# Kernel optimization log

Hardware: AMD Instinct MI355X
Metric: run time of the kernel (lower is better)

## Reference

```python
import jax, jax.numpy as jnp
import numpy as np

N = 50000      # nodes
E = 800000     # edges
F = 128        # num_features
H = 128        # hidden_channels
L = 3          # num_layers
P = 32         # num_partitions
EPS = 1e-5     # BatchNorm1d eps


def _batchnorm(h):
    # BatchNorm1d(affine=False, track_running_stats=False): batch stats, biased var
    m = jnp.mean(h, axis=0)
    v = jnp.var(h, axis=0)
    return (h - m) * jax.lax.rsqrt(v + EPS)


def setup_inputs() -> dict:
    key = jax.random.key(0)
    ks = jax.random.split(key, 12)
    x = jax.random.normal(ks[0], (N, F), dtype=jnp.float32)
    edge_index = jax.random.randint(ks[1], (2, E), 0, N)
    edge_weights = jax.random.uniform(ks[2], (E,), dtype=jnp.float32)
    partitions = (jax.random.uniform(ks[3], (N, P)) < (1.0 / P)).astype(jnp.float32)
    node_weights = jax.random.uniform(ks[4], (N,), dtype=jnp.float32)
    edge_curr_node = jax.random.uniform(ks[5], (N,), dtype=jnp.float32)
    conv_w = 0.05 * jax.random.normal(ks[6], (L, F, H), dtype=jnp.float32)
    conv_b = jnp.zeros((L, H), dtype=jnp.float32)
    lin1_w = 0.05 * jax.random.normal(ks[7], (4 * H, H), dtype=jnp.float32)
    lin1_b = jnp.zeros((H,), dtype=jnp.float32)
    lin2_w = 0.05 * jax.random.normal(ks[8], (H, 1), dtype=jnp.float32)
    lin2_b = jnp.zeros((1,), dtype=jnp.float32)
    return {"x": x, "edge_index": edge_index, "edge_weights": edge_weights,
            "partitions": partitions, "node_weights": node_weights,
            "edge_curr_node": edge_curr_node, "conv_w": conv_w, "conv_b": conv_b,
            "lin1_w": lin1_w, "lin1_b": lin1_b, "lin2_w": lin2_w,
            "lin2_b": lin2_b, "curr_node_id": 123}


def reference(x, edge_index, edge_weights, partitions, node_weights,
              edge_curr_node, conv_w, conv_b, lin1_w, lin1_b, lin2_w, lin2_b,
              curr_node_id):
    src, dst = edge_index[0], edge_index[1]
    # GCN normalization with added self-loops (weight 1)
    deg = jax.ops.segment_sum(edge_weights, dst, num_segments=N) + 1.0
    dinv = jax.lax.rsqrt(deg)
    norm = dinv[src] * edge_weights * dinv[dst]          # [E]
    self_norm = (dinv * dinv)[:, None]                   # [N,1]

    h = x
    for l in range(L):
        hw = h @ conv_w[l] + conv_b[l]                   # [N,H]
        agg = jax.ops.segment_sum(hw[src] * norm[:, None], dst, num_segments=N)
        agg = agg + hw * self_norm                       # self-loop term
        h = jax.nn.relu(_batchnorm(agg))

    x_curr = h[curr_node_id]                             # [H]
    # mlp scoring: concat [h | x_curr | edge_col repeated to 2H] -> [N,4H]
    cat = jnp.concatenate([
        h,
        jnp.broadcast_to(x_curr[None, :], (N, H)),
        jnp.broadcast_to(edge_curr_node[:, None], (N, 2 * H)),
    ], axis=1)
    scores = jax.nn.relu(cat @ lin1_w + lin1_b) @ lin2_w + lin2_b  # [N,1]
    # pool == 'sum'
    partition_scores = scores.T @ partitions             # [1,P]
    return (partition_scores, h)
```

## Files before the change

kernel.cpp:

```cpp
#include <hip/hip_runtime.h>

#define N_NODES 50000
#define N_EDGES 800000
#define NP 50048
#define MAXDEG 64
#define PADK 136
#define NCOPY 64
#define WPB 512
#define NBUK 196
#define BCAP 6144
#define EBB 782

typedef __bf16 bf16_8 __attribute__((ext_vector_type(8)));
typedef float  f32_4  __attribute__((ext_vector_type(4)));

__device__ inline float2 bf2f2(unsigned int u) {
    union { unsigned int i; float f; } a, b;
    a.i = u << 16;
    b.i = u & 0xffff0000u;
    return make_float2(a.f, b.f);
}

__global__ void k_init_wprep(float* __restrict__ colpart, float* __restrict__ out_head,
                             const float* __restrict__ conv_w, const float* __restrict__ lin1_w,
                             __bf16* __restrict__ WT, float* __restrict__ svec,
                             int* __restrict__ bcnt) {
    int b = blockIdx.x, t = threadIdx.x;
    if (b < WPB) {
        int mat = b >> 7, n = b & 127;
        if (t < 128) {
            const float* srcm = (mat < 3) ? (conv_w + (size_t)mat * 16384) : lin1_w;
            WT[((size_t)mat * 128 + n) * 128 + t] = (__bf16)srcm[(size_t)t * 128 + n];
        }
    } else if (b == WPB) {
        if (t < 128) {
            float s = 0.f;
            for (int k = 256; k < 512; ++k) s += lin1_w[(size_t)k * 128 + t];
            svec[t] = s;
        }
    } else if (b < WPB + 65) {
        int i = (b - WPB - 1) * 256 + t;
        colpart[i] = 0.f;
    } else {
        if (t < 32) out_head[t] = 0.f;
        for (int i = t; i < NBUK * 16; i += 256) bcnt[i] = 0;
    }
}

__global__ __launch_bounds__(1024) void k_bucket(const int* __restrict__ src,
                                                 const int* __restrict__ dst,
                                                 const float* __restrict__ ew,
                                                 int* __restrict__ bcnt,
                                                 uint2* __restrict__ ebuf) {
    __shared__ uint2 stage[1024];
    __shared__ int cnt[NBUK], cnt2[NBUK], lstart[NBUK], gb[NBUK];
    __shared__ int wtot[4];
    int t = threadIdx.x;
    int e0 = blockIdx.x * 1024;
    int tot = min(1024, N_EDGES - e0);
    if (t < NBUK) { cnt[t] = 0; cnt2[t] = 0; }
    __syncthreads();
    uint2 rec = make_uint2(0u, 0u); int b = -1;
    if (t < tot) {
        int e = e0 + t;
        unsigned s = (unsigned)src[e], d = (unsigned)dst[e];
        rec = make_uint2(s | (d << 16), __float_as_uint(ew[e]));
        b = (int)(d >> 8);
        atomicAdd(&cnt[b], 1);
    }
    __syncthreads();
    int c = (t < NBUK) ? cnt[t] : 0;
    int x = c;
#pragma unroll
    for (int d2 = 1; d2 < 64; d2 <<= 1) {
        int v = __shfl_up(x, d2, 64);
        if ((t & 63) >= d2) x += v;
    }
    if ((t & 63) == 63 && t < 256) wtot[t >> 6] = x;
    if (t < NBUK && c > 0) gb[t] = atomicAdd(&bcnt[t * 16], c);
    __syncthreads();
    if (t < NBUK) {
        int pre = x - c;
        for (int w = 0; w < (t >> 6); ++w) pre += wtot[w];
        lstart[t] = pre;
    }
    __syncthreads();
    if (t < tot) {
        int r = atomicAdd(&cnt2[b], 1);
        stage[lstart[b] + r] = rec;
    }
    __syncthreads();
    if (t < tot) {
        uint2 v = stage[t];
        int bb = (int)(v.x >> 24);
        int idx = gb[bb] + (t - lstart[bb]);
        if (idx < BCAP) ebuf[(size_t)bb * BCAP + idx] = v;
    }
}

__global__ __launch_bounds__(256) void k_build(const int* __restrict__ bcnt,
                                               const uint2* __restrict__ ebuf,
                                               uint2* __restrict__ packed,
                                               int* __restrict__ rowofs,
                                               int* __restrict__ fillp,
                                               float* __restrict__ dinv) {
    __shared__ int cnt[256];
    __shared__ float wsum[256];
    __shared__ int pos[256];
    __shared__ int wtot[4];
    int t = threadIdx.x, b = blockIdx.x;
    cnt[t] = 0; wsum[t] = 0.f;
    __syncthreads();
    int m = min(bcnt[b * 16], BCAP);
    for (int i = t; i < m; i += 256) {
        uint2 rec = ebuf[(size_t)b * BCAP + i];
        int local = (int)(rec.x >> 16) & 255;
        atomicAdd(&cnt[local], 1);
        atomicAdd(&wsum[local], __uint_as_float(rec.y));
    }
    __syncthreads();
    int c = cnt[t];
    int x = c;
#pragma unroll
    for (int d2 = 1; d2 < 64; d2 <<= 1) {
        int v = __shfl_up(x, d2, 64);
        if ((t & 63) >= d2) x += v;
    }
    if ((t & 63) == 63) wtot[t >> 6] = x;
    __syncthreads();
    int pre = x - c;
    for (int w = 0; w < (t >> 6); ++w) pre += wtot[w];
    int rstart = b * BCAP + pre;
    pos[t] = rstart;
    __syncthreads();
    for (int i = t; i < m; i += 256) {
        uint2 rec = ebuf[(size_t)b * BCAP + i];
        int local = (int)(rec.x >> 16) & 255;
        int p = atomicAdd(&pos[local], 1);
        packed[p] = make_uint2(rec.x & 0xffffu, rec.y);
    }
    int gn = b * 256 + t;
    if (gn < N_NODES) {
        fillp[gn] = c;
        rowofs[gn] = rstart;
        dinv[gn] = rsqrtf(1.0f + wsum[t]);
    }
}

template <int AMODE>
__global__ __launch_bounds__(256) void k_gemm_mfma(const float* __restrict__ A,
                                                   const float* __restrict__ mean,
                                                   const float* __restrict__ rstd,
                                                   const __bf16* __restrict__ WT,
                                                   const float* __restrict__ bias,
                                                   __bf16* __restrict__ C, int nrows,
                                                   uint2* __restrict__ packed,
                                                   const int* __restrict__ rowofs,
                                                   const int* __restrict__ fillp,
                                                   const float* __restrict__ dinv,
                                                   int gemmBlocks) {
    __shared__ __bf16 As[64 * PADK];
    __shared__ __bf16 Ws[128 * PADK];
    int t = threadIdx.x;
    if (AMODE == 0 && blockIdx.x >= gemmBlocks) {
        int n = ((blockIdx.x - gemmBlocks) * 256 + t) >> 6;
        int lane = t & 63;
        if (n >= N_NODES) return;
        int num = min(fillp[n], MAXDEG);
        if (lane < num) {
            int ro = rowofs[n];
            uint2 e = packed[ro + lane];
            float w = dinv[(int)e.x] * __uint_as_float(e.y) * dinv[n];
            packed[ro + lane] = make_uint2(e.x, __float_as_uint(w));
        }
        return;
    }
    int rowBase = blockIdx.x * 64;
    const uint4* WTg = (const uint4*)WT;
    for (int i = t; i < 2048; i += 256) {
        int n = i >> 4, k8 = i & 15;
        *(uint4*)&Ws[n * PADK + k8 * 8] = WTg[i];
    }
    const float4* A4 = (const float4*)A;
    const float4* M4 = (const float4*)mean;
    const float4* R4 = (const float4*)rstd;
    for (int i = t; i < 1024; i += 256) {
        int r = i >> 4, k8 = i & 15;
        int gr = rowBase + r;
        float4 a0 = make_float4(0.f, 0.f, 0.f, 0.f), a1 = a0;
        if (gr < nrows) {
            a0 = A4[(size_t)gr * 32 + k8 * 2];
            a1 = A4[(size_t)gr * 32 + k8 * 2 + 1];
        }
        if (AMODE == 1) {
            float4 m0 = M4[k8 * 2], m1 = M4[k8 * 2 + 1];
            float4 r0 = R4[k8 * 2], r1 = R4[k8 * 2 + 1];
            a0.x = fmaxf((a0.x - m0.x) * r0.x, 0.f); a0.y = fmaxf((a0.y - m0.y) * r0.y, 0.f);
            a0.z = fmaxf((a0.z - m0.z) * r0.z, 0.f); a0.w = fmaxf((a0.w - m0.w) * r0.w, 0.f);
            a1.x = fmaxf((a1.x - m1.x) * r1.x, 0.f); a1.y = fmaxf((a1.y - m1.y) * r1.y, 0.f);
            a1.z = fmaxf((a1.z - m1.z) * r1.z, 0.f); a1.w = fmaxf((a1.w - m1.w) * r1.w, 0.f);
        }
        bf16_8 o = { (__bf16)a0.x, (__bf16)a0.y, (__bf16)a0.z, (__bf16)a0.w,
                     (__bf16)a1.x, (__bf16)a1.y, (__bf16)a1.z, (__bf16)a1.w };
        *(bf16_8*)&As[r * PADK + k8 * 8] = o;
    }
    __syncthreads();
    int wave = t >> 6, lane = t & 63, quad = lane >> 4, m = lane & 15;
    int ar = wave * 16 + m;
    f32_4 acc[8];
#pragma unroll
    for (int i = 0; i < 8; ++i) acc[i] = (f32_4){0.f, 0.f, 0.f, 0.f};
#pragma unroll
    for (int kk = 0; kk < 4; ++kk) {
        bf16_8 a = *(const bf16_8*)&As[ar * PADK + kk * 32 + quad * 8];
#pragma unroll
        for (int n0 = 0; n0 < 8; ++n0) {
            bf16_8 b = *(const bf16_8*)&Ws[(n0 * 16 + m) * PADK + kk * 32 + quad * 8];
            acc[n0] = __builtin_amdgcn_mfma_f32_16x16x32_bf16(a, b, acc[n0], 0, 0, 0);
        }
    }
    __syncthreads();
#pragma unroll
    for (int n0 = 0; n0 < 8; ++n0) {
        int col = n0 * 16 + m;
        float bi = bias[col];
#pragma unroll
        for (int r = 0; r < 4; ++r) {
            int rr = wave * 16 + quad * 4 + r;
            As[rr * PADK + col] = (__bf16)(acc[n0][r] + bi);
        }
    }
    __syncthreads();
    uint4* Cg = (uint4*)C;
    for (int i = t; i < 1024; i += 256) {
        int r = i >> 4, k8 = i & 15;
        int gr = rowBase + r;
        if (gr < nrows) Cg[(size_t)gr * 16 + k8] = *(const uint4*)&As[r * PADK + k8 * 8];
    }
}

__global__ __launch_bounds__(256) void k_agg(const __bf16* __restrict__ hwb,
                                             const uint2* __restrict__ packed,
                                             const int* __restrict__ rowofs,
                                             const int* __restrict__ fillp,
                                             const float* __restrict__ dinv,
                                             float* __restrict__ agg,
                                             float* __restrict__ colpart) {
    __shared__ float red1[4 * 128], red2[4 * 128];
    int t = threadIdx.x;
    int n = (blockIdx.x * 256 + t) >> 6;
    int lane = t & 63, wave = t >> 6;
    int rs = lane >> 4, c16 = lane & 15;
    float acc[8];
#pragma unroll
    for (int k = 0; k < 8; ++k) acc[k] = 0.f;
    const uint4* hwq = (const uint4*)hwb;
    if (n < N_NODES) {
        int num = min(fillp[n], MAXDEG);
        int ro = rowofs[n];
        float dvn = dinv[n];
        uint4 sv = hwq[(size_t)n * 16 + c16];
        int s_l = 0; float w_l = 0.f;
        if (lane < num) {
            uint2 e = packed[ro + lane];
            s_l = (int)e.x;
            w_l = __uint_as_float(e.y);
        }
        int groups = (num + 3) >> 2;
        int g = 0;
        for (; g + 4 <= groups; g += 4) {
            uint4 u[4]; float w[4];
#pragma unroll
            for (int j = 0; j < 4; ++j) {
                int idx = (g + j) * 4 + rs;
                int s = __shfl(s_l, idx, 64);
                w[j] = __shfl(w_l, idx, 64);
                u[j] = hwq[(size_t)s * 16 + c16];
            }
#pragma unroll
            for (int j = 0; j < 4; ++j) {
                float2 f0 = bf2f2(u[j].x), f1 = bf2f2(u[j].y);
                float2 f2 = bf2f2(u[j].z), f3 = bf2f2(u[j].w);
                acc[0] += f0.x * w[j]; acc[1] += f0.y * w[j];
                acc[2] += f1.x * w[j]; acc[3] += f1.y * w[j];
                acc[4] += f2.x * w[j]; acc[5] += f2.y * w[j];
                acc[6] += f3.x * w[j]; acc[7] += f3.y * w[j];
            }
        }
        for (; g < groups; ++g) {
            int idx = g * 4 + rs;
            int s = __shfl(s_l, idx, 64);
            float w = __shfl(w_l, idx, 64);
            uint4 u = hwq[(size_t)s * 16 + c16];
            float2 f0 = bf2f2(u.x), f1 = bf2f2(u.y), f2 = bf2f2(u.z), f3 = bf2f2(u.w);
            acc[0] += f0.x * w; acc[1] += f0.y * w;
            acc[2] += f1.x * w; acc[3] += f1.y * w;
            acc[4] += f2.x * w; acc[5] += f2.y * w;
            acc[6] += f3.x * w; acc[7] += f3.y * w;
        }
#pragma unroll
        for (int k = 0; k < 8; ++k) {
            acc[k] += __shfl_xor(acc[k], 16, 64);
            acc[k] += __shfl_xor(acc[k], 32, 64);
        }
        float d2 = dvn * dvn;
        float2 s0 = bf2f2(sv.x), s1 = bf2f2(sv.y), s2 = bf2f2(sv.z), s3 = bf2f2(sv.w);
        acc[0] += s0.x * d2; acc[1] += s0.y * d2;
        acc[2] += s1.x * d2; acc[3] += s1.y * d2;
        acc[4] += s2.x * d2; acc[5] += s2.y * d2;
        acc[6] += s3.x * d2; acc[7] += s3.y * d2;
        if (rs < 2) {
            float4 o = make_float4(acc[rs * 4 + 0], acc[rs * 4 + 1],
                                   acc[rs * 4 + 2], acc[rs * 4 + 3]);
            ((float4*)agg)[(size_t)n * 32 + c16 * 2 + rs] = o;
        }
    }
    if (rs == 0) {
        *(float4*)&red1[wave * 128 + c16 * 8 + 0] =
            make_float4(acc[0], acc[1], acc[2], acc[3]);
        *(float4*)&red1[wave * 128 + c16 * 8 + 4] =
            make_float4(acc[4], acc[5], acc[6], acc[7]);
        *(float4*)&red2[wave * 128 + c16 * 8 + 0] =
            make_float4(acc[0] * acc[0], acc[1] * acc[1], acc[2] * acc[2], acc[3] * acc[3]);
        *(float4*)&red2[wave * 128 + c16 * 8 + 4] =
            make_float4(acc[4] * acc[4], acc[5] * acc[5], acc[6] * acc[6], acc[7] * acc[7]);
    }
    __syncthreads();
    if (t < 128) {
        float s = red1[t] + red1[128 + t] + red1[256 + t] + red1[384 + t];
        float q = red2[t] + red2[128 + t] + red2[256 + t] + red2[384 + t];
        int c = blockIdx.x & (NCOPY - 1);
        unsafeAtomicAdd(&colpart[c * 128 + t], s);
        unsafeAtomicAdd(&colpart[NCOPY * 128 + c * 128 + t], q);
    }
}

__global__ void k_bnfinal(float* colpart, float* mean, float* rstd) {
    int j = threadIdx.x;
    float s = 0.f, q = 0.f;
    for (int c = 0; c < NCOPY; ++c) {
        s += colpart[c * 128 + j];
        q += colpart[NCOPY * 128 + c * 128 + j];
        colpart[c * 128 + j] = 0.f;
        colpart[NCOPY * 128 + c * 128 + j] = 0.f;
    }
    float m = s * (1.0f / N_NODES);
    float v = q * (1.0f / N_NODES) - m * m;
    mean[j] = m;
    rstd[j] = rsqrtf(v + 1e-5f);
}

__global__ void k_prep(const float* __restrict__ agg, const float* __restrict__ mean,
                       const float* __restrict__ rstd, const int* __restrict__ cid,
                       const float* __restrict__ lin1w, const float* __restrict__ lin1b,
                       float* c0) {
    __shared__ float xc[128];
    int t = threadIdx.x;
    int cn = cid[0];
    float a = agg[(size_t)cn * 128 + t];
    xc[t] = fmaxf((a - mean[t]) * rstd[t], 0.f);
    __syncthreads();
    float acc = lin1b[t];
    for (int k = 0; k < 128; ++k)
        acc += xc[k] * lin1w[(size_t)(128 + k) * 128 + t];
    c0[t] = acc;
}

__global__ __launch_bounds__(256) void k_score_mfma(const float* __restrict__ agg,
                                                    const float* __restrict__ mean,
                                                    const float* __restrict__ rstd,
                                                    const __bf16* __restrict__ WT,
                                                    const float* __restrict__ c0,
                                                    const float* __restrict__ svec,
                                                    const float* __restrict__ ecn,
                                                    const float* __restrict__ lin2w,
                                                    const float* __restrict__ lin2b,
                                                    float* __restrict__ scores,
                                                    float* __restrict__ hout,
                                                    int nrows) {
    __shared__ __bf16 As[64 * PADK];
    __shared__ __bf16 Ws[128 * PADK];
    __shared__ float c0s[128], svs[128], l2s[128];
    int t = threadIdx.x;
    int rowBase = blockIdx.x * 64;
    const uint4* WTg = (const uint4*)WT;
    for (int i = t; i < 2048; i += 256) {
        int n = i >> 4, k8 = i & 15;
        *(uint4*)&Ws[n * PADK + k8 * 8] = WTg[i];
    }
    const float4* A4 = (const float4*)agg;
    const float4* M4 = (const float4*)mean;
    const float4* R4 = (const float4*)rstd;
    float4* H4 = (float4*)hout;
    for (int i = t; i < 1024; i += 256) {
        int r = i >> 4, k8 = i & 15;
        int gr = rowBase + r;
        float4 a0 = make_float4(0.f, 0.f, 0.f, 0.f), a1 = a0;
        if (gr < nrows) {
            a0 = A4[(size_t)gr * 32 + k8 * 2];
            a1 = A4[(size_t)gr * 32 + k8 * 2 + 1];
        }
        float4 m0 = M4[k8 * 2], m1 = M4[k8 * 2 + 1];
        float4 r0 = R4[k8 * 2], r1 = R4[k8 * 2 + 1];
        float4 f0, f1;
        f0.x = fmaxf((a0.x - m0.x) * r0.x, 0.f); f0.y = fmaxf((a0.y - m0.y) * r0.y, 0.f);
        f0.z = fmaxf((a0.z - m0.z) * r0.z, 0.f); f0.w = fmaxf((a0.w - m0.w) * r0.w, 0.f);
        f1.x = fmaxf((a1.x - m1.x) * r1.x, 0.f); f1.y = fmaxf((a1.y - m1.y) * r1.y, 0.f);
        f1.z = fmaxf((a1.z - m1.z) * r1.z, 0.f); f1.w = fmaxf((a1.w - m1.w) * r1.w, 0.f);
        if (gr < nrows) {
            H4[(size_t)gr * 32 + k8 * 2] = f0;
            H4[(size_t)gr * 32 + k8 * 2 + 1] = f1;
        }
        bf16_8 o = { (__bf16)f0.x, (__bf16)f0.y, (__bf16)f0.z, (__bf16)f0.w,
                     (__bf16)f1.x, (__bf16)f1.y, (__bf16)f1.z, (__bf16)f1.w };
        *(bf16_8*)&As[r * PADK + k8 * 8] = o;
    }
    if (t < 128) { c0s[t] = c0[t]; svs[t] = svec[t]; l2s[t] = lin2w[t]; }
    __syncthreads();
    int wave = t >> 6, lane = t & 63, quad = lane >> 4, m = lane & 15;
    int ar = wave * 16 + m;
    f32_4 acc[8];
#pragma unroll
    for (int i = 0; i < 8; ++i) acc[i] = (f32_4){0.f, 0.f, 0.f, 0.f};
#pragma unroll
    for (int kk = 0; kk < 4; ++kk) {
        bf16_8 a = *(const bf16_8*)&As[ar * PADK + kk * 32 + quad * 8];
#pragma unroll
        for (int n0 = 0; n0 < 8; ++n0) {
            bf16_8 b = *(const bf16_8*)&Ws[(n0 * 16 + m) * PADK + kk * 32 + quad * 8];
            acc[n0] = __builtin_amdgcn_mfma_f32_16x16x32_bf16(a, b, acc[n0], 0, 0, 0);
        }
    }
    float l2b = lin2b[0];
#pragma unroll
    for (int r = 0; r < 4; ++r) {
        int row = rowBase + wave * 16 + quad * 4 + r;
        float e = (row < nrows) ? ecn[row] : 0.f;
        float partial = 0.f;
#pragma unroll
        for (int n0 = 0; n0 < 8; ++n0) {
            int col = n0 * 16 + m;
            float v = acc[n0][r] + c0s[col] + e * svs[col];
            partial += fmaxf(v, 0.f) * l2s[col];
        }
        partial += __shfl_xor(partial, 8, 16);
        partial += __shfl_xor(partial, 4, 16);
        partial += __shfl_xor(partial, 2, 16);
        partial += __shfl_xor(partial, 1, 16);
        if (m == 0 && row < nrows) scores[row] = partial + l2b;
    }
}

__global__ void k_partition(const float* __restrict__ scores, const float* __restrict__ part,
                            float* out) {
    __shared__ float red[256];
    int t = threadIdx.x;
    int p = t & 31, rg = t >> 5;
    float acc = 0.f;
    for (int r = blockIdx.x * 8 + rg; r < N_NODES; r += gridDim.x * 8)
        acc += scores[r] * part[(size_t)r * 32 + p];
    red[t] = acc;
    __syncthreads();
    if (t < 32) {
        float s = 0.f;
        for (int i = 0; i < 8; ++i) s += red[i * 32 + t];
        unsafeAtomicAdd(&out[t], s);
    }
}

extern "C" void kernel_launch(void* const* d_in, const int* in_sizes, int n_in,
                              void* d_out, int out_size, void* d_ws, size_t ws_size,
                              hipStream_t stream) {
    const float* x        = (const float*)d_in[0];
    const int*   eidx     = (const int*)d_in[1];
    const float* ew       = (const float*)d_in[2];
    const float* parts    = (const float*)d_in[3];
    const float* ecn      = (const float*)d_in[5];
    const float* conv_w   = (const float*)d_in[6];
    const float* conv_b   = (const float*)d_in[7];
    const float* lin1_w   = (const float*)d_in[8];
    const float* lin1_b   = (const float*)d_in[9];
    const float* lin2_w   = (const float*)d_in[10];
    const float* lin2_b   = (const float*)d_in[11];
    const int*   cid      = (const int*)d_in[12];

    const int* src = eidx;
    const int* dst = eidx + N_EDGES;

    char* p = (char*)d_ws;
    auto alloc = [&](size_t bytes) { char* r = p; p += (bytes + 255) & ~size_t(255); return r; };
    int*    fillp   = (int*)alloc((size_t)NP * 4);
    int*    rowofs  = (int*)alloc((size_t)NP * 4);
    uint2*  packed  = (uint2*)alloc((size_t)NBUK * BCAP * 8);
    float*  dinv    = (float*)alloc(NP * 4);
    float*  scores  = (float*)alloc(NP * 4);
    float*  colpart = (float*)alloc(2 * NCOPY * 128 * 4);
    float*  mean    = (float*)alloc(128 * 4);
    float*  rstd    = (float*)alloc(128 * 4);
    float*  c0      = (float*)alloc(128 * 4);
    float*  svec    = (float*)alloc(128 * 4);
    __bf16* WT      = (__bf16*)alloc(4 * 128 * 128 * 2);
    __bf16* hwb     = (__bf16*)alloc((size_t)N_NODES * 128 * 2);
    float*  agg     = (float*)alloc((size_t)N_NODES * 128 * 4);
    int*    bcnt    = (int*)alloc((size_t)NBUK * 16 * 4);
    uint2*  ebuf    = (uint2*)alloc((size_t)NBUK * BCAP * 8);

    float* out_head = (float*)d_out;
    float* hbuf     = (float*)d_out + 32;

    const int GB = (N_NODES + 63) / 64;
    const int AB = (N_NODES * 64 + 255) / 256;

    k_init_wprep<<<WPB + 66, 256, 0, stream>>>(colpart, out_head, conv_w, lin1_w, WT, svec, bcnt);
    k_bucket<<<EBB, 1024, 0, stream>>>(src, dst, ew, bcnt, ebuf);
    k_build<<<NBUK, 256, 0, stream>>>(bcnt, ebuf, packed, rowofs, fillp, dinv);

    for (int l = 0; l < 3; ++l) {
        if (l == 0)
            k_gemm_mfma<0><<<GB + AB, 256, 0, stream>>>(x, mean, rstd, WT, conv_b, hwb, N_NODES,
                                                        packed, rowofs, fillp, dinv, GB);
        else
            k_gemm_mfma<1><<<GB, 256, 0, stream>>>(agg, mean, rstd, WT + (size_t)l * 16384,
                                                   conv_b + (size_t)l * 128, hwb, N_NODES,
                                                   nullptr, nullptr, nullptr, nullptr, GB);
        k_agg<<<AB, 256, 0, stream>>>(hwb, packed, rowofs, fillp, dinv, agg, colpart);
        k_bnfinal<<<1, 128, 0, stream>>>(colpart, mean, rstd);
    }

    k_prep<<<1, 128, 0, stream>>>(agg, mean, rstd, cid, lin1_w, lin1_b, c0);
    k_score_mfma<<<GB, 256, 0, stream>>>(agg, mean, rstd, WT + (size_t)3 * 16384, c0, svec,
                                         ecn, lin2_w, lin2_b, scores, hbuf, N_NODES);
    k_partition<<<256, 256, 0, stream>>>(scores, parts, out_head);
}
```

Baseline: 354.3 us.

## Fold BN finalize, query-node prep and partition pooling into consumer kernels

```diff
diff --git a/kernel.cpp b/kernel.cpp
--- a/kernel.cpp
+++ b/kernel.cpp
@@ -6,6 +6,7 @@
 #define MAXDEG 64
 #define PADK 136
 #define NCOPY 64
+#define CPSZ (2 * NCOPY * 128)
 #define WPB 512
 #define NBUK 196
 #define BCAP 6144
@@ -38,7 +39,7 @@
             for (int k = 256; k < 512; ++k) s += lin1_w[(size_t)k * 128 + t];
             svec[t] = s;
         }
-    } else if (b < WPB + 65) {
+    } else if (b < WPB + 1 + 192) {
         int i = (b - WPB - 1) * 256 + t;
         colpart[i] = 0.f;
     } else {
@@ -149,8 +150,7 @@
 
 template <int AMODE>
 __global__ __launch_bounds__(256) void k_gemm_mfma(const float* __restrict__ A,
-                                                   const float* __restrict__ mean,
-                                                   const float* __restrict__ rstd,
+                                                   const float* __restrict__ colpart,
                                                    const __bf16* __restrict__ WT,
                                                    const float* __restrict__ bias,
                                                    __bf16* __restrict__ C, int nrows,
@@ -161,6 +161,7 @@
                                                    int gemmBlocks) {
     __shared__ __bf16 As[64 * PADK];
     __shared__ __bf16 Ws[128 * PADK];
+    __shared__ float meanS[128], rstdS[128];
     int t = threadIdx.x;
     if (AMODE == 0 && blockIdx.x >= gemmBlocks) {
         int n = ((blockIdx.x - gemmBlocks) * 256 + t) >> 6;
@@ -175,6 +176,20 @@
         }
         return;
     }
+    if (AMODE == 1) {
+        if (t < 128) {
+            float s = 0.f, q = 0.f;
+            for (int c = 0; c < NCOPY; ++c) {
+                s += colpart[c * 128 + t];
+                q += colpart[NCOPY * 128 + c * 128 + t];
+            }
+            float mm = s * (1.0f / N_NODES);
+            float vv = q * (1.0f / N_NODES) - mm * mm;
+            meanS[t] = mm;
+            rstdS[t] = rsqrtf(vv + 1e-5f);
+        }
+        __syncthreads();
+    }
     int rowBase = blockIdx.x * 64;
     const uint4* WTg = (const uint4*)WT;
     for (int i = t; i < 2048; i += 256) {
@@ -182,8 +197,6 @@
         *(uint4*)&Ws[n * PADK + k8 * 8] = WTg[i];
     }
     const float4* A4 = (const float4*)A;
-    const float4* M4 = (const float4*)mean;
-    const float4* R4 = (const float4*)rstd;
     for (int i = t; i < 1024; i += 256) {
         int r = i >> 4, k8 = i & 15;
         int gr = rowBase + r;
@@ -193,8 +206,10 @@
             a1 = A4[(size_t)gr * 32 + k8 * 2 + 1];
         }
         if (AMODE == 1) {
-            float4 m0 = M4[k8 * 2], m1 = M4[k8 * 2 + 1];
-            float4 r0 = R4[k8 * 2], r1 = R4[k8 * 2 + 1];
+            float4 m0 = *(const float4*)&meanS[k8 * 8];
+            float4 m1 = *(const float4*)&meanS[k8 * 8 + 4];
+            float4 r0 = *(const float4*)&rstdS[k8 * 8];
+            float4 r1 = *(const float4*)&rstdS[k8 * 8 + 4];
             a0.x = fmaxf((a0.x - m0.x) * r0.x, 0.f); a0.y = fmaxf((a0.y - m0.y) * r0.y, 0.f);
             a0.z = fmaxf((a0.z - m0.z) * r0.z, 0.f); a0.w = fmaxf((a0.w - m0.w) * r0.w, 0.f);
             a1.x = fmaxf((a1.x - m1.x) * r1.x, 0.f); a1.y = fmaxf((a1.y - m1.y) * r1.y, 0.f);
@@ -335,62 +350,61 @@
     }
 }
 
-__global__ void k_bnfinal(float* colpart, float* mean, float* rstd) {
-    int j = threadIdx.x;
-    float s = 0.f, q = 0.f;
-    for (int c = 0; c < NCOPY; ++c) {
-        s += colpart[c * 128 + j];
-        q += colpart[NCOPY * 128 + c * 128 + j];
-        colpart[c * 128 + j] = 0.f;
-        colpart[NCOPY * 128 + c * 128 + j] = 0.f;
-    }
-    float m = s * (1.0f / N_NODES);
-    float v = q * (1.0f / N_NODES) - m * m;
-    mean[j] = m;
-    rstd[j] = rsqrtf(v + 1e-5f);
-}
-
-__global__ void k_prep(const float* __restrict__ agg, const float* __restrict__ mean,
-                       const float* __restrict__ rstd, const int* __restrict__ cid,
-                       const float* __restrict__ lin1w, const float* __restrict__ lin1b,
-                       float* c0) {
-    __shared__ float xc[128];
-    int t = threadIdx.x;
-    int cn = cid[0];
-    float a = agg[(size_t)cn * 128 + t];
-    xc[t] = fmaxf((a - mean[t]) * rstd[t], 0.f);
-    __syncthreads();
-    float acc = lin1b[t];
-    for (int k = 0; k < 128; ++k)
-        acc += xc[k] * lin1w[(size_t)(128 + k) * 128 + t];
-    c0[t] = acc;
-}
-
 __global__ __launch_bounds__(256) void k_score_mfma(const float* __restrict__ agg,
-                                                    const float* __restrict__ mean,
-                                                    const float* __restrict__ rstd,
+                                                    const float* __restrict__ colpart,
                                                     const __bf16* __restrict__ WT,
-                                                    const float* __restrict__ c0,
                                                     const float* __restrict__ svec,
                                                     const float* __restrict__ ecn,
                                                     const float* __restrict__ lin2w,
                                                     const float* __restrict__ lin2b,
-                                                    float* __restrict__ scores,
+                                                    const float* __restrict__ part,
+                                                    float* __restrict__ out,
                                                     float* __restrict__ hout,
+                                                    const int* __restrict__ cid,
+                                                    const float* __restrict__ lin1w,
+                                                    const float* __restrict__ lin1b,
                                                     int nrows) {
     __shared__ __bf16 As[64 * PADK];
     __shared__ __bf16 Ws[128 * PADK];
-    __shared__ float c0s[128], svs[128], l2s[128];
+    __shared__ float meanS[128], rstdS[128], xc[128], c0p[128];
+    __shared__ float c0s[128], svs[128], l2s[128], sc[64];
     int t = threadIdx.x;
     int rowBase = blockIdx.x * 64;
+    if (t < 128) {
+        float s = 0.f, q = 0.f;
+        for (int c = 0; c < NCOPY; ++c) {
+            s += colpart[c * 128 + t];
+            q += colpart[NCOPY * 128 + c * 128 + t];
+        }
+        float mm = s * (1.0f / N_NODES);
+        float vv = q * (1.0f / N_NODES) - mm * mm;
+        meanS[t] = mm;
+        rstdS[t] = rsqrtf(vv + 1e-5f);
+    }
+    __syncthreads();
+    if (t < 128) {
+        int cn = cid[0];
+        float a = agg[(size_t)cn * 128 + t];
+        xc[t] = fmaxf((a - meanS[t]) * rstdS[t], 0.f);
+        svs[t] = svec[t]; l2s[t] = lin2w[t];
+    }
+    __syncthreads();
+    {
+        int col = t & 127, half = t >> 7;
+        float a = 0.f;
+#pragma unroll 8
+        for (int k = half * 64; k < half * 64 + 64; ++k)
+            a += xc[k] * lin1w[(size_t)(128 + k) * 128 + col];
+        if (half) c0p[col] = a;
+        __syncthreads();
+        if (!half) c0s[col] = a + c0p[col] + lin1b[col];
+    }
     const uint4* WTg = (const uint4*)WT;
     for (int i = t; i < 2048; i += 256) {
         int n = i >> 4, k8 = i & 15;
         *(uint4*)&Ws[n * PADK + k8 * 8] = WTg[i];
     }
     const float4* A4 = (const float4*)agg;
-    const float4* M4 = (const float4*)mean;
-    const float4* R4 = (const float4*)rstd;
     float4* H4 = (float4*)hout;
     for (int i = t; i < 1024; i += 256) {
         int r = i >> 4, k8 = i & 15;
@@ -400,8 +414,10 @@
             a0 = A4[(size_t)gr * 32 + k8 * 2];
             a1 = A4[(size_t)gr * 32 + k8 * 2 + 1];
         }
-        float4 m0 = M4[k8 * 2], m1 = M4[k8 * 2 + 1];
-        float4 r0 = R4[k8 * 2], r1 = R4[k8 * 2 + 1];
+        float4 m0 = *(const float4*)&meanS[k8 * 8];
+        float4 m1 = *(const float4*)&meanS[k8 * 8 + 4];
+        float4 r0 = *(const float4*)&rstdS[k8 * 8];
+        float4 r1 = *(const float4*)&rstdS[k8 * 8 + 4];
         float4 f0, f1;
         f0.x = fmaxf((a0.x - m0.x) * r0.x, 0.f); f0.y = fmaxf((a0.y - m0.y) * r0.y, 0.f);
         f0.z = fmaxf((a0.z - m0.z) * r0.z, 0.f); f0.w = fmaxf((a0.w - m0.w) * r0.w, 0.f);
@@ -415,7 +431,6 @@
                      (__bf16)f1.x, (__bf16)f1.y, (__bf16)f1.z, (__bf16)f1.w };
         *(bf16_8*)&As[r * PADK + k8 * 8] = o;
     }
-    if (t < 128) { c0s[t] = c0[t]; svs[t] = svec[t]; l2s[t] = lin2w[t]; }
     __syncthreads();
     int wave = t >> 6, lane = t & 63, quad = lane >> 4, m = lane & 15;
     int ar = wave * 16 + m;
@@ -447,23 +462,15 @@
         partial += __shfl_xor(partial, 4, 16);
         partial += __shfl_xor(partial, 2, 16);
         partial += __shfl_xor(partial, 1, 16);
-        if (m == 0 && row < nrows) scores[row] = partial + l2b;
-    }
-}
-
-__global__ void k_partition(const float* __restrict__ scores, const float* __restrict__ part,
-                            float* out) {
-    __shared__ float red[256];
-    int t = threadIdx.x;
-    int p = t & 31, rg = t >> 5;
-    float acc = 0.f;
-    for (int r = blockIdx.x * 8 + rg; r < N_NODES; r += gridDim.x * 8)
-        acc += scores[r] * part[(size_t)r * 32 + p];
-    red[t] = acc;
+        if (m == 0) sc[wave * 16 + quad * 4 + r] = (row < nrows) ? partial + l2b : 0.f;
+    }
     __syncthreads();
     if (t < 32) {
         float s = 0.f;
-        for (int i = 0; i < 8; ++i) s += red[i * 32 + t];
+        for (int r2 = 0; r2 < 64; ++r2) {
+            int row = rowBase + r2;
+            if (row < nrows) s += sc[r2] * part[(size_t)row * 32 + t];
+        }
         unsafeAtomicAdd(&out[t], s);
     }
 }
@@ -493,11 +500,7 @@
     int*    rowofs  = (int*)alloc((size_t)NP * 4);
     uint2*  packed  = (uint2*)alloc((size_t)NBUK * BCAP * 8);
     float*  dinv    = (float*)alloc(NP * 4);
-    float*  scores  = (float*)alloc(NP * 4);
-    float*  colpart = (float*)alloc(2 * NCOPY * 128 * 4);
-    float*  mean    = (float*)alloc(128 * 4);
-    float*  rstd    = (float*)alloc(128 * 4);
-    float*  c0      = (float*)alloc(128 * 4);
+    float*  colpart = (float*)alloc((size_t)3 * CPSZ * 4);
     float*  svec    = (float*)alloc(128 * 4);
     __bf16* WT      = (__bf16*)alloc(4 * 128 * 128 * 2);
     __bf16* hwb     = (__bf16*)alloc((size_t)N_NODES * 128 * 2);
@@ -511,24 +514,24 @@
     const int GB = (N_NODES + 63) / 64;
     const int AB = (N_NODES * 64 + 255) / 256;
 
-    k_init_wprep<<<WPB + 66, 256, 0, stream>>>(colpart, out_head, conv_w, lin1_w, WT, svec, bcnt);
+    k_init_wprep<<<WPB + 194, 256, 0, stream>>>(colpart, out_head, conv_w, lin1_w, WT, svec, bcnt);
     k_bucket<<<EBB, 1024, 0, stream>>>(src, dst, ew, bcnt, ebuf);
     k_build<<<NBUK, 256, 0, stream>>>(bcnt, ebuf, packed, rowofs, fillp, dinv);
 
     for (int l = 0; l < 3; ++l) {
         if (l == 0)
-            k_gemm_mfma<0><<<GB + AB, 256, 0, stream>>>(x, mean, rstd, WT, conv_b, hwb, N_NODES,
+            k_gemm_mfma<0><<<GB + AB, 256, 0, stream>>>(x, nullptr, WT, conv_b, hwb, N_NODES,
                                                         packed, rowofs, fillp, dinv, GB);
         else
-            k_gemm_mfma<1><<<GB, 256, 0, stream>>>(agg, mean, rstd, WT + (size_t)l * 16384,
+            k_gemm_mfma<1><<<GB, 256, 0, stream>>>(agg, colpart + (size_t)(l - 1) * CPSZ,
+                                                   WT + (size_t)l * 16384,
                                                    conv_b + (size_t)l * 128, hwb, N_NODES,
                                                    nullptr, nullptr, nullptr, nullptr, GB);
-        k_agg<<<AB, 256, 0, stream>>>(hwb, packed, rowofs, fillp, dinv, agg, colpart);
-        k_bnfinal<<<1, 128, 0, stream>>>(colpart, mean, rstd);
-    }
-
-    k_prep<<<1, 128, 0, stream>>>(agg, mean, rstd, cid, lin1_w, lin1_b, c0);
-    k_score_mfma<<<GB, 256, 0, stream>>>(agg, mean, rstd, WT + (size_t)3 * 16384, c0, svec,
-                                         ecn, lin2_w, lin2_b, scores, hbuf, N_NODES);
-    k_partition<<<256, 256, 0, stream>>>(scores, parts, out_head);
-}
+        k_agg<<<AB, 256, 0, stream>>>(hwb, packed, rowofs, fillp, dinv, agg,
+                                      colpart + (size_t)l * CPSZ);
+    }
+
+    k_score_mfma<<<GB, 256, 0, stream>>>(agg, colpart + (size_t)2 * CPSZ,
+                                         WT + (size_t)3 * 16384, svec, ecn, lin2_w, lin2_b,
+                                         parts, out_head, hbuf, cid, lin1_w, lin1_b, N_NODES);
+}
```

New measurement: 386.4 us. 9.1% more time.
